# Optimization experiments

Measured on AMD Instinct MI355X. Metric: run time of the kernel, lower is better.

## Reference

```python
import jax, jax.numpy as jnp
import numpy as np

D = 768

def setup_inputs() -> dict:
    key = jax.random.key(0)
    k1, k2, k3, k4, k5 = jax.random.split(key, 5)
    query = jax.random.normal(k1, (32, 1024, D), dtype=jnp.float32)
    key_t = jax.random.normal(k2, (32, 1024, D), dtype=jnp.float32)
    w1 = jax.random.normal(k3, (1, D), dtype=jnp.float32) * 0.02
    w2 = jax.random.normal(k4, (1, D), dtype=jnp.float32) * 0.02
    w3 = jax.random.normal(k5, (1, D), dtype=jnp.float32) * 0.02
    return {"query": query, "key": key_t, "w1": w1, "w2": w2, "w3": w3}

def reference(query, key, w1, w2, w3):
    # q_logit: [B, Lq, 1], k_logit: [B, Lk, 1] -> transposed to [B, 1, Lk]
    q_logit = query @ w1[0]                       # [B, Lq]
    k_logit = key @ w2[0]                         # [B, Lk]
    dot_logit = jnp.einsum('bqd,bkd->bqk', query, w3[0] * key)  # [B, Lq, Lk]
    return q_logit[:, :, None] + k_logit[:, None, :] + dot_logit
```

## Files before the change

### kernel.cpp

```cpp
#include <hip/hip_runtime.h>
#include <hip/hip_bf16.h>

#define BB 32
#define LL 1024
#define DD 768

typedef short bf16x8 __attribute__((ext_vector_type(8)));
typedef float f32x4 __attribute__((ext_vector_type(4)));

__device__ __forceinline__ unsigned short f2bf(float f) {
    unsigned u = __builtin_bit_cast(unsigned, f);
    u += 0x7fffu + ((u >> 16) & 1u);
    return (unsigned short)(u >> 16);
}

__global__ __launch_bounds__(256) void convert_kernel(
    const float* __restrict__ Q, const float* __restrict__ K,
    const float* __restrict__ w1, const float* __restrict__ w2,
    const float* __restrict__ w3,
    unsigned short* __restrict__ Qb, unsigned short* __restrict__ Kb,
    float* __restrict__ qlog, float* __restrict__ klog)
{
    const int ln  = threadIdx.x & 63;
    const int row = blockIdx.x * 4 + (threadIdx.x >> 6);
    const size_t base = (size_t)row * DD;

    float qdot = 0.f, kdot = 0.f;
    #pragma unroll
    for (int c = 0; c < 3; ++c) {
        const int idx = c * 64 + ln;
        float4 qv  = ((const float4*)(Q + base))[idx];
        float4 kv  = ((const float4*)(K + base))[idx];
        float4 w1v = ((const float4*)w1)[idx];
        float4 w2v = ((const float4*)w2)[idx];
        float4 w3v = ((const float4*)w3)[idx];

        qdot += qv.x*w1v.x + qv.y*w1v.y + qv.z*w1v.z + qv.w*w1v.w;
        kdot += kv.x*w2v.x + kv.y*w2v.y + kv.z*w2v.z + kv.w*w2v.w;

        ushort4 pq, pk;
        pq.x = f2bf(qv.x); pq.y = f2bf(qv.y); pq.z = f2bf(qv.z); pq.w = f2bf(qv.w);
        pk.x = f2bf(kv.x * w3v.x); pk.y = f2bf(kv.y * w3v.y);
        pk.z = f2bf(kv.z * w3v.z); pk.w = f2bf(kv.w * w3v.w);
        ((ushort4*)(Qb + base))[idx] = pq;
        ((ushort4*)(Kb + base))[idx] = pk;
    }

    #pragma unroll
    for (int off = 32; off > 0; off >>= 1) {
        qdot += __shfl_down(qdot, off, 64);
        kdot += __shfl_down(kdot, off, 64);
    }
    if (ln == 0) { qlog[row] = qdot; klog[row] = kdot; }
}

__global__ __launch_bounds__(256) void trilinear_gemm(
    const unsigned short* __restrict__ Qb, const unsigned short* __restrict__ Kb,
    const float* __restrict__ qlog, const float* __restrict__ klog,
    float* __restrict__ out)
{
    __shared__ __align__(16) unsigned short As[128 * 32];
    __shared__ __align__(16) unsigned short Bs[128 * 32];

    const int tid  = threadIdx.x;
    const int w    = tid >> 6, lane = tid & 63;
    const int wq   = w >> 1, wk = w & 1;

    const int id = blockIdx.x;
    const int g  = id & 7;
    const int j  = id >> 3;
    const int b  = g + ((j >> 6) << 3);
    const int t0 = j & 63;
    const int qt = t0 >> 3, kt = t0 & 7;

    const unsigned short* Ag = Qb + ((size_t)b * LL + qt * 128) * DD;
    const unsigned short* Bg = Kb + ((size_t)b * LL + kt * 128) * DD;

    const int srow  = lane >> 2;
    const int scol  = ((lane & 3) ^ ((lane >> 3) & 3)) * 8;
    const int m    = lane & 15;
    const int l    = lane >> 4;
    const int p8   = (l ^ ((m >> 1) & 3)) * 8;

    f32x4 acc[4][4] = {};

    for (int k0 = 0; k0 < DD; k0 += 32) {
        __syncthreads();
        #pragma unroll
        for (int j2 = 0; j2 < 2; ++j2) {
            const int r = w * 32 + j2 * 16 + srow;
            __builtin_amdgcn_global_load_lds(
                (const __attribute__((address_space(1))) void*)(Ag + (size_t)r * DD + k0 + scol),
                (__attribute__((address_space(3))) void*)&As[(w * 32 + j2 * 16) * 32],
                16, 0, 0);
            __builtin_amdgcn_global_load_lds(
                (const __attribute__((address_space(1))) void*)(Bg + (size_t)r * DD + k0 + scol),
                (__attribute__((address_space(3))) void*)&Bs[(w * 32 + j2 * 16) * 32],
                16, 0, 0);
        }
        __syncthreads();

        bf16x8 av[4], bv[4];
        #pragma unroll
        for (int tt = 0; tt < 4; ++tt) {
            av[tt] = *(const bf16x8*)&As[(wq * 64 + tt * 16 + m) * 32 + p8];
            bv[tt] = *(const bf16x8*)&Bs[(wk * 64 + tt * 16 + m) * 32 + p8];
        }
        #pragma unroll
        for (int at = 0; at < 4; ++at)
            #pragma unroll
            for (int bt = 0; bt < 4; ++bt)
                acc[at][bt] = __builtin_amdgcn_mfma_f32_16x16x32_bf16(
                    av[at], bv[bt], acc[at][bt], 0, 0, 0);
    }

    const int qrow0 = qt * 128 + wq * 64;
    const int kcol0 = kt * 128 + wk * 64;
    const float* ql = qlog + b * LL + qrow0;
    const float* kl = klog + b * LL + kcol0;
    float* outp = out + ((size_t)b * LL + qrow0) * LL + kcol0;
    const int col = lane & 15, r4 = (lane >> 4) * 4;

    #pragma unroll
    for (int at = 0; at < 4; ++at) {
        #pragma unroll
        for (int bt = 0; bt < 4; ++bt) {
            const float klv = kl[bt * 16 + col];
            #pragma unroll
            for (int r = 0; r < 4; ++r) {
                const int row = at * 16 + r4 + r;
                outp[(size_t)row * LL + bt * 16 + col] = acc[at][bt][r] + ql[row] + klv;
            }
        }
    }
}

extern "C" void kernel_launch(void* const* d_in, const int* in_sizes, int n_in,
                              void* d_out, int out_size, void* d_ws, size_t ws_size,
                              hipStream_t stream) {
    const float* Q  = (const float*)d_in[0];
    const float* K  = (const float*)d_in[1];
    const float* w1 = (const float*)d_in[2];
    const float* w2 = (const float*)d_in[3];
    const float* w3 = (const float*)d_in[4];
    float* out = (float*)d_out;

    unsigned short* Qb = (unsigned short*)d_ws;
    unsigned short* Kb = Qb + (size_t)BB * LL * DD;
    float* qlog = (float*)(Kb + (size_t)BB * LL * DD);
    float* klog = qlog + BB * LL;

    convert_kernel<<<BB * LL / 4, 256, 0, stream>>>(Q, K, w1, w2, w3, Qb, Kb, qlog, klog);
    trilinear_gemm<<<2048, 256, 0, stream>>>(Qb, Kb, qlog, klog, out);
}
```

Before: 356.5 us.

## Triple-buffer LDS tiles to overlap global loads with MFMA compute

Replaces the single-buffered LDS K-loop, which synced twice per step, with a three-stage ring of LDS buffers. Tiles are prefetched two steps ahead and the loop uses manual vmcnt waits plus a single barrier per iteration, so global-to-LDS loads overlap with MFMA work. This is meant to hide global memory latency in the GEMM. It triples LDS use (48 KB per block), which may lower occupancy, and correctness depends on the hand-counted vmcnt values.

```diff
diff --git a/kernel.cpp b/kernel.cpp
--- a/kernel.cpp
+++ b/kernel.cpp
@@ -59,8 +59,8 @@
     const float* __restrict__ qlog, const float* __restrict__ klog,
     float* __restrict__ out)
 {
-    __shared__ __align__(16) unsigned short As[128 * 32];
-    __shared__ __align__(16) unsigned short Bs[128 * 32];
+    __shared__ __align__(16) unsigned short As[3][128 * 32];
+    __shared__ __align__(16) unsigned short Bs[3][128 * 32];
 
     const int tid  = threadIdx.x;
     const int w    = tid >> 6, lane = tid & 63;
@@ -84,35 +84,70 @@
 
     f32x4 acc[4][4] = {};
 
-    for (int k0 = 0; k0 < DD; k0 += 32) {
-        __syncthreads();
-        #pragma unroll
-        for (int j2 = 0; j2 < 2; ++j2) {
-            const int r = w * 32 + j2 * 16 + srow;
-            __builtin_amdgcn_global_load_lds(
-                (const __attribute__((address_space(1))) void*)(Ag + (size_t)r * DD + k0 + scol),
-                (__attribute__((address_space(3))) void*)&As[(w * 32 + j2 * 16) * 32],
-                16, 0, 0);
-            __builtin_amdgcn_global_load_lds(
-                (const __attribute__((address_space(1))) void*)(Bg + (size_t)r * DD + k0 + scol),
-                (__attribute__((address_space(3))) void*)&Bs[(w * 32 + j2 * 16) * 32],
-                16, 0, 0);
-        }
-        __syncthreads();
+    #define STAGE(kt_, s_) do {                                                  \
+        const int k0_ = (kt_) * 32;                                              \
+        _Pragma("unroll")                                                        \
+        for (int j2 = 0; j2 < 2; ++j2) {                                         \
+            const int rb_ = w * 32 + j2 * 16;         \
+            __builtin_amdgcn_global_load_lds(                                    \
+                (const __attribute__((address_space(1))) void*)                  \
+                    (Ag + (size_t)(rb_ + srow) * DD + k0_ + scol),               \
+                (__attribute__((address_space(3))) void*)&As[s_][rb_ * 32],      \
+                16, 0, 0);                                                       \
+            __builtin_amdgcn_global_load_lds(                                    \
+                (const __attribute__((address_space(1))) void*)                  \
+                    (Bg + (size_t)(rb_ + srow) * DD + k0_ + scol),               \
+                (__attribute__((address_space(3))) void*)&Bs[s_][rb_ * 32],      \
+                16, 0, 0);                                                       \
+        }                                                                        \
+    } while (0)
 
-        bf16x8 av[4], bv[4];
-        #pragma unroll
-        for (int tt = 0; tt < 4; ++tt) {
-            av[tt] = *(const bf16x8*)&As[(wq * 64 + tt * 16 + m) * 32 + p8];
-            bv[tt] = *(const bf16x8*)&Bs[(wk * 64 + tt * 16 + m) * 32 + p8];
-        }
-        #pragma unroll
-        for (int at = 0; at < 4; ++at)
-            #pragma unroll
-            for (int bt = 0; bt < 4; ++bt)
-                acc[at][bt] = __builtin_amdgcn_mfma_f32_16x16x32_bf16(
-                    av[at], bv[bt], acc[at][bt], 0, 0, 0);
+    #define COMPUTE(s_) do {                                                     \
+        const unsigned short* A_ = As[s_];                                       \
+        const unsigned short* B_ = Bs[s_];                                       \
+        bf16x8 av[4], bv[4];                                                     \
+        _Pragma("unroll")                                                        \
+        for (int tt = 0; tt < 4; ++tt) {                                         \
+            av[tt] = *(const bf16x8*)&A_[(wq * 64 + tt * 16 + m) * 32 + p8];     \
+            bv[tt] = *(const bf16x8*)&B_[(wk * 64 + tt * 16 + m) * 32 + p8];     \
+        }                                                                        \
+        asm volatile("s_waitcnt lgkmcnt(0)" ::: "memory");                       \
+        __builtin_amdgcn_sched_barrier(0);                                       \
+        _Pragma("unroll")                                                        \
+        for (int at = 0; at < 4; ++at)                                           \
+            _Pragma("unroll")                                                    \
+            for (int bt = 0; bt < 4; ++bt)                                       \
+                acc[at][bt] = __builtin_amdgcn_mfma_f32_16x16x32_bf16(           \
+                    av[at], bv[bt], acc[at][bt], 0, 0, 0);                       \
+    } while (0)
+
+    const int NT = DD / 32;
+
+    STAGE(0, 0);
+    STAGE(1, 1);
+    asm volatile("s_waitcnt vmcnt(4)" ::: "memory");
+    __builtin_amdgcn_s_barrier();
+    __builtin_amdgcn_sched_barrier(0);
+
+    int bc = 0, bs = 2;
+    for (int t = 0; t < NT - 2; ++t) {
+        STAGE(t + 2, bs);
+        COMPUTE(bc);
+        asm volatile("s_waitcnt vmcnt(4)" ::: "memory");
+        __builtin_amdgcn_s_barrier();
+        __builtin_amdgcn_sched_barrier(0);
+        bc = (bc == 2) ? 0 : bc + 1;
+        bs = (bs == 2) ? 0 : bs + 1;
     }
+    COMPUTE(bc);
+    asm volatile("s_waitcnt vmcnt(0)" ::: "memory");
+    __builtin_amdgcn_s_barrier();
+    __builtin_amdgcn_sched_barrier(0);
+    bc = (bc == 2) ? 0 : bc + 1;
+    COMPUTE(bc);
+
+    #undef STAGE
+    #undef COMPUTE
 
     const int qrow0 = qt * 128 + wq * 64;
     const int kcol0 = kt * 128 + wk * 64;
```

Result: no change. 359.5 us (+0.8%).
